# Optimization experiments

Hardware: AMD Instinct MI355X
Metric: run time of the kernel (lower is better)

## Reference

```python
import jax, jax.numpy as jnp
import numpy as np

NEG = -9e15
ALPHA = 0.2  # leaky relu slope

def setup_inputs() -> dict:
    key = jax.random.key(0)
    k1, k2, k3, k4 = jax.random.split(key, 4)
    N, Fin, Fout = 8192, 512, 256
    h = jax.random.normal(k1, (N, Fin), dtype=jnp.float32)
    adj = jax.random.randint(k2, (N, N), 0, 2, dtype=jnp.int32)
    # xavier_uniform with gain=1.414
    gain = 1.414
    limW = gain * np.sqrt(6.0 / (Fin + Fout))
    W = jax.random.uniform(k3, (Fin, Fout), dtype=jnp.float32, minval=-limW, maxval=limW)
    lima = gain * np.sqrt(6.0 / (2 * Fout + 1))
    a = jax.random.uniform(k4, (2 * Fout, 1), dtype=jnp.float32, minval=-lima, maxval=lima)
    return {"h": h, "adj": adj, "W": W, "a": a}

def reference(h, adj, W, a):
    Fout = W.shape[1]
    Wh = h @ W                                   # [N, Fout]
    # decompose a = [a1; a2]: e_ij = leaky(a1.Wh_i + a2.Wh_j)
    f1 = Wh @ a[:Fout]                           # [N, 1]
    f2 = Wh @ a[Fout:]                           # [N, 1]
    e = jax.nn.leaky_relu(f1 + f2.T, negative_slope=ALPHA)  # [N, N]
    e = jnp.where(adj > 0, e, jnp.float32(NEG))
    attention = jax.nn.softmax(e, axis=1)
    # dropout is identity at inference (training=False)
    h_prime = attention @ Wh                     # [N, Fout]
    return jax.nn.elu(h_prime)
```

## Files before the change

### kernel.cpp

```cpp
#include <hip/hip_runtime.h>
#include <cstdint>
#include <cstddef>

#define ALPHA 0.2f

typedef __attribute__((ext_vector_type(8)))  short short8;
typedef __attribute__((ext_vector_type(16))) float f32x16;

static __device__ __forceinline__ unsigned short f2bf(float x) {
  union { float f; unsigned u; } c; c.f = x;
  unsigned u = c.u;
  unsigned r = (u + 0x7FFFu + ((u >> 16) & 1u)) >> 16;
  return (unsigned short)r;
}

__global__ __launch_bounds__(256, 2) void gemm1(const float* __restrict__ h,
                                                const float* __restrict__ W,
                                                float* __restrict__ Wh) {
  __shared__ float As[32][132];
  __shared__ float Bs[32][64];
  const int t = threadIdx.x;
  const int bid = blockIdx.x;
  const int nb = bid & 3, mb = bid >> 2;
  const int m0 = mb * 128, n0 = nb * 64;
  const int ty = t >> 4, tx = t & 15;
  float acc[8][4];
#pragma unroll
  for (int i = 0; i < 8; i++)
#pragma unroll
    for (int j = 0; j < 4; j++) acc[i][j] = 0.f;

  for (int k0 = 0; k0 < 512; k0 += 32) {
#pragma unroll
    for (int c = 0; c < 4; c++) {
      int m = c * 32 + (t >> 3);
      int kq = (t & 7) * 4;
      float4 v = *(const float4*)&h[(size_t)(m0 + m) * 512 + k0 + kq];
      As[kq + 0][m] = v.x; As[kq + 1][m] = v.y;
      As[kq + 2][m] = v.z; As[kq + 3][m] = v.w;
    }
#pragma unroll
    for (int c = 0; c < 2; c++) {
      int k = c * 16 + (t >> 4);
      int n = (t & 15) * 4;
      *(float4*)&Bs[k][n] = *(const float4*)&W[(size_t)(k0 + k) * 256 + n0 + n];
    }
    __syncthreads();
#pragma unroll
    for (int k = 0; k < 32; k++) {
      float4 a0 = *(float4*)&As[k][ty * 8];
      float4 a1 = *(float4*)&As[k][ty * 8 + 4];
      float4 b  = *(float4*)&Bs[k][tx * 4];
      float av[8] = {a0.x, a0.y, a0.z, a0.w, a1.x, a1.y, a1.z, a1.w};
      float bv[4] = {b.x, b.y, b.z, b.w};
#pragma unroll
      for (int i = 0; i < 8; i++)
#pragma unroll
        for (int j = 0; j < 4; j++) acc[i][j] = fmaf(av[i], bv[j], acc[i][j]);
    }
    __syncthreads();
  }
#pragma unroll
  for (int i = 0; i < 8; i++) {
    float4 v = {acc[i][0], acc[i][1], acc[i][2], acc[i][3]};
    *(float4*)&Wh[(size_t)(m0 + ty * 8 + i) * 256 + n0 + tx * 4] = v;
  }
}

__global__ __launch_bounds__(256) void rowstats(const float* __restrict__ Wh,
                                                const float* __restrict__ a,
                                                float* __restrict__ f1,
                                                float* __restrict__ f2,
                                                unsigned* __restrict__ uvpack) {
  const int t = threadIdx.x;
  const int w = t >> 6, lane = t & 63;
  const int i = blockIdx.x * 4 + w;
  float4 wv = *(const float4*)&Wh[(size_t)i * 256 + lane * 4];
  float4 a1 = *(const float4*)&a[lane * 4];
  float4 a2 = *(const float4*)&a[256 + lane * 4];
  float s1 = wv.x * a1.x + wv.y * a1.y + wv.z * a1.z + wv.w * a1.w;
  float s2 = wv.x * a2.x + wv.y * a2.y + wv.z * a2.z + wv.w * a2.w;
#pragma unroll
  for (int off = 32; off; off >>= 1) { s1 += __shfl_xor(s1, off); s2 += __shfl_xor(s2, off); }
  if (lane == 0) {
    f1[i] = s1; f2[i] = s2;
    float u = __expf(s2), v = __expf(ALPHA * s2);
    uvpack[i] = (unsigned)f2bf(u) | ((unsigned)f2bf(v) << 16);
  }
}

__global__ __launch_bounds__(256) void wtrans(const float* __restrict__ Wh,
                                              unsigned short* __restrict__ WhT) {
  __shared__ unsigned short T[64][80];
  const int t = threadIdx.x;
  const int bi = blockIdx.x & 127;
  const int bc = blockIdx.x >> 7;
  const int i0 = bi * 64, c0 = bc * 64;
  {
    const int il = t >> 2, cq = (t & 3) * 16;
#pragma unroll
    for (int k = 0; k < 4; ++k) {
      float4 v = *(const float4*)&Wh[(size_t)(i0 + il) * 256 + c0 + cq + k * 4];
      T[cq + k * 4 + 0][il] = f2bf(v.x);
      T[cq + k * 4 + 1][il] = f2bf(v.y);
      T[cq + k * 4 + 2][il] = f2bf(v.z);
      T[cq + k * 4 + 3][il] = f2bf(v.w);
    }
  }
  __syncthreads();
  {
    const int cl = t >> 2, iq = (t & 3) * 16;
    *(uint4*)&WhT[(size_t)(c0 + cl) * 8192 + i0 + iq]     = *(const uint4*)&T[cl][iq];
    *(uint4*)&WhT[(size_t)(c0 + cl) * 8192 + i0 + iq + 8] = *(const uint4*)&T[cl][iq + 8];
  }
}

__global__ __launch_bounds__(256) void f2max_k(const float* __restrict__ f2,
                                               float* __restrict__ f2maxp) {
  __shared__ float red[256];
  const int t = threadIdx.x;
  float m = -1e30f;
  for (int c = 0; c < 32; c++) m = fmaxf(m, f2[c * 256 + t]);
  red[t] = m;
  __syncthreads();
  for (int s = 128; s; s >>= 1) {
    if (t < s) red[t] = fmaxf(red[t], red[t + s]);
    __syncthreads();
  }
  if (t == 0) f2maxp[0] = red[0];
}

__global__ __launch_bounds__(256) void maskpack(const int* __restrict__ adj,
                                                unsigned long long* __restrict__ mask) {
  __shared__ unsigned long long mbuf[4][128];
  const int t = threadIdx.x, wave = t >> 6, lane = t & 63;
  const int row = blockIdx.x * 4 + wave;
  const int* ap = adj + (size_t)row * 8192 + lane;
#pragma unroll 1
  for (int it0 = 0; it0 < 128; it0 += 4) {
    int a0 = ap[(it0 + 0) * 64];
    int a1 = ap[(it0 + 1) * 64];
    int a2 = ap[(it0 + 2) * 64];
    int a3 = ap[(it0 + 3) * 64];
    unsigned long long b0 = __ballot(a0 > 0);
    unsigned long long b1 = __ballot(a1 > 0);
    unsigned long long b2 = __ballot(a2 > 0);
    unsigned long long b3 = __ballot(a3 > 0);
    if (lane == 0) {
      mbuf[wave][it0 + 0] = b0; mbuf[wave][it0 + 1] = b1;
      mbuf[wave][it0 + 2] = b2; mbuf[wave][it0 + 3] = b3;
    }
  }
  __syncthreads();
  uint4* dst = (uint4*)(mask + (size_t)blockIdx.x * 4 * 128);
  dst[t] = ((const uint4*)mbuf)[t];
}

#define ATTN_SUB(KSUB, MWORD, UCA, UCB, BFC, BFN, SCUR)                          \
  {                                                                              \
    const unsigned mbyte_ = ((MWORD) >> (((KSUB) & 1) * 16 + aselsh)) & 0xFFu;   \
    const unsigned uu_[8] = {UCA.x, UCA.y, UCA.z, UCA.w, UCB.x, UCB.y, UCB.z, UCB.w}; \
    float w_[8];                                                                 \
    _Pragma("unroll")                                                            \
    for (int jj = 0; jj < 8; jj++) {                                             \
      union { unsigned u; float f; } cu_, cv_;                                   \
      cu_.u = uu_[jj] << 16;                                                     \
      cv_.u = uu_[jj] & 0xFFFF0000u;                                             \
      float wv_ = (cu_.f > Ui) ? Ai * cu_.f : Bi * cv_.f;                        \
      int ext_ = ((int)(mbyte_ << (31 - jj))) >> 31;    \
      union { float f; int i; } wu_; wu_.f = wv_; wu_.i &= ext_;                 \
      w_[jj] = wu_.f;                                                            \
    }                                                                            \
    lpriv += ((w_[0] + w_[1]) + (w_[2] + w_[3])) + ((w_[4] + w_[5]) + (w_[6] + w_[7])); \
    union { uint4 q; short8 s; } af_;                                            \
    asm("v_cvt_pk_bf16_f32 %0, %1, %2" : "=v"(af_.q.x) : "v"(w_[0]), "v"(w_[1]));\
    asm("v_cvt_pk_bf16_f32 %0, %1, %2" : "=v"(af_.q.y) : "v"(w_[2]), "v"(w_[3]));\
    asm("v_cvt_pk_bf16_f32 %0, %1, %2" : "=v"(af_.q.z) : "v"(w_[4]), "v"(w_[5]));\
    asm("v_cvt_pk_bf16_f32 %0, %1, %2" : "=v"(af_.q.w) : "v"(w_[6]), "v"(w_[7]));\
    const int sn_ = (SCUR) + 1 < 128 ? (SCUR) + 1 : 127;                         \
    _Pragma("unroll")                                                            \
    for (int ct = 0; ct < 8; ct++)                                               \
      BFN[ct] = *(const short8*)(wtp + (size_t)ct * (32 * 8192) + (size_t)sn_ * 16); \
    _Pragma("unroll")                                                            \
    for (int ct = 0; ct < 8; ct++)                                               \
      acc[ct] = __builtin_amdgcn_mfma_f32_32x32x16_bf16(af_.s, BFC[ct], acc[ct], 0, 0, 0); \
  }

#define ATTN_GROUP(G, UC, UN, MC, MN)                                            \
  {                                                                              \
    const int gn_ = (G) < 31 ? (G) + 1 : 31;                                     \
    MN = mp[gn_];                                                                \
    UN[0] = *(const uint4*)(uvp + gn_ * 64 + 0);                                 \
    UN[1] = *(const uint4*)(uvp + gn_ * 64 + 4);                                 \
    ATTN_SUB(0, MC.x, UC[0], UC[1], bfA, bfB, 4 * (G) + 0);                      \
    UN[2] = *(const uint4*)(uvp + gn_ * 64 + 16);                                \
    UN[3] = *(const uint4*)(uvp + gn_ * 64 + 20);                                \
    ATTN_SUB(1, MC.x, UC[2], UC[3], bfB, bfA, 4 * (G) + 1);                      \
    UN[4] = *(const uint4*)(uvp + gn_ * 64 + 32);                                \
    UN[5] = *(const uint4*)(uvp + gn_ * 64 + 36);                                \
    ATTN_SUB(2, MC.y, UC[4], UC[5], bfA, bfB, 4 * (G) + 2);                      \
    UN[6] = *(const uint4*)(uvp + gn_ * 64 + 48);                                \
    UN[7] = *(const uint4*)(uvp + gn_ * 64 + 52);                                \
    ATTN_SUB(3, MC.y, UC[6], UC[7], bfB, bfA, 4 * (G) + 3);                      \
  }

__global__ __launch_bounds__(256, 1) void attn_main(const unsigned long long* __restrict__ maskw,
                                                    const float* __restrict__ f1,
                                                    const unsigned* __restrict__ uvpack,
                                                    const unsigned short* __restrict__ WhT,
                                                    const float* __restrict__ f2maxp,
                                                    float* __restrict__ out) {
  __shared__ float red[4][32][260];
  __shared__ float lsum[4][32];
  const int t = threadIdx.x;
  const int wave = t >> 6, lane = t & 63;
  const int am = lane & 31, asel = lane >> 5;
  const int aselsh = asel * 8;
  const int r0 = blockIdx.x * 32;
  const int row = r0 + am;
  const int jq = wave * 2048;

  const float F2max = f2maxp[0];
  const float f1v = f1[row];
  const float x = f1v + F2max;
  const float M = x > 0.f ? x : ALPHA * x;
  const float Ai = __expf(f1v - M);
  const float Bi = __expf(ALPHA * f1v - M);
  const float Ui = __expf(-f1v);

  f32x16 acc[8] = {};
  const uint2* mp = (const uint2*)maskw + (size_t)row * 128 + wave * 32;
  const unsigned* uvp = uvpack + jq + aselsh;
  const unsigned short* wtp = WhT + (size_t)am * 8192 + jq + aselsh;

  uint2 mg = mp[0], mgN;
  uint4 ug[8], ugN[8];
#pragma unroll
  for (int k = 0; k < 4; k++) {
    ug[2 * k]     = *(const uint4*)(uvp + k * 16);
    ug[2 * k + 1] = *(const uint4*)(uvp + k * 16 + 4);
  }
  short8 bfA[8], bfB[8];
#pragma unroll
  for (int ct = 0; ct < 8; ct++)
    bfA[ct] = *(const short8*)(wtp + (size_t)ct * (32 * 8192));
  float lpriv = 0.f;

#pragma unroll 1
  for (int gg = 0; gg < 16; ++gg) {
    ATTN_GROUP(2 * gg,     ug,  ugN, mg,  mgN);
    ATTN_GROUP(2 * gg + 1, ugN, ug,  mgN, mg);
  }

#pragma unroll
  for (int ct = 0; ct < 8; ct++) {
#pragma unroll
    for (int reg = 0; reg < 16; reg++) {
      const int rowl = (reg & 3) + 8 * (reg >> 2) + 4 * asel;
      red[wave][rowl][ct * 32 + am] = acc[ct][reg];
    }
  }
  lpriv += __shfl_xor(lpriv, 32);
  if (asel == 0) lsum[wave][am] = lpriv;
  __syncthreads();

  const int rr = t >> 3, cb = (t & 7) * 32;
  const float l = lsum[0][rr] + lsum[1][rr] + lsum[2][rr] + lsum[3][rr];
  const float inv = 1.0f / fmaxf(l, 1e-30f);
#pragma unroll
  for (int cc = 0; cc < 32; cc += 4) {
    float4 v;
    v.x = red[0][rr][cb + cc + 0] + red[1][rr][cb + cc + 0] + red[2][rr][cb + cc + 0] + red[3][rr][cb + cc + 0];
    v.y = red[0][rr][cb + cc + 1] + red[1][rr][cb + cc + 1] + red[2][rr][cb + cc + 1] + red[3][rr][cb + cc + 1];
    v.z = red[0][rr][cb + cc + 2] + red[1][rr][cb + cc + 2] + red[2][rr][cb + cc + 2] + red[3][rr][cb + cc + 2];
    v.w = red[0][rr][cb + cc + 3] + red[1][rr][cb + cc + 3] + red[2][rr][cb + cc + 3] + red[3][rr][cb + cc + 3];
    v.x *= inv; v.y *= inv; v.z *= inv; v.w *= inv;
    float4 o;
    o.x = v.x > 0.f ? v.x : __expf(v.x) - 1.f;
    o.y = v.y > 0.f ? v.y : __expf(v.y) - 1.f;
    o.z = v.z > 0.f ? v.z : __expf(v.z) - 1.f;
    o.w = v.w > 0.f ? v.w : __expf(v.w) - 1.f;
    *(float4*)&out[(size_t)(r0 + rr) * 256 + cb + cc] = o;
  }
}

extern "C" void kernel_launch(void* const* d_in, const int* in_sizes, int n_in,
                              void* d_out, int out_size, void* d_ws, size_t ws_size,
                              hipStream_t stream) {
  const float* h  = (const float*)d_in[0];
  const int* adj  = (const int*)d_in[1];
  const float* W  = (const float*)d_in[2];
  const float* a  = (const float*)d_in[3];
  float* out = (float*)d_out;
  char* ws = (char*)d_ws;

  float* Wh            = (float*)ws;
  unsigned long long* mask = (unsigned long long*)(ws + (size_t)(8u << 20));
  unsigned short* WhT  = (unsigned short*)(ws + (size_t)(16u << 20));
  float* f1            = (float*)(ws + (size_t)(20u << 20));
  float* f2            = (float*)(ws + (size_t)(20u << 20) + (32u << 10));
  unsigned* uvpack     = (unsigned*)(ws + (size_t)(20u << 20) + (64u << 10));
  float* f2maxp        = (float*)(ws + (size_t)(20u << 20) + (96u << 10));

  maskpack<<<2048, 256, 0, stream>>>(adj, mask);
  gemm1<<<256, 256, 0, stream>>>(h, W, Wh);
  rowstats<<<2048, 256, 0, stream>>>(Wh, a, f1, f2, uvpack);
  wtrans<<<512, 256, 0, stream>>>(Wh, WhT);
  f2max_k<<<1, 256, 0, stream>>>(f2, f2maxp);
  attn_main<<<256, 256, 0, stream>>>(mask, f1, uvpack, WhT, f2maxp, out);
}
```

Before: 553.6 us.

## Split attention work across waves by output columns instead of key ranges

Each wave now computes 64 output columns over the full 8192-key range instead of all 256 columns over a quarter of the keys. This removes the large LDS cross-wave reduction buffer, the __syncthreads, and the per-wave accumulator array, and writes outputs straight from registers. In exchange, every wave recomputes the masked softmax weights for all keys, quadrupling that ALU work and the mask/uv loads per block, and the output stores become scalar and less coalesced.

```diff
diff --git a/kernel.cpp b/kernel.cpp
--- a/kernel.cpp
+++ b/kernel.cpp
@@ -177,18 +177,16 @@
     asm("v_cvt_pk_bf16_f32 %0, %1, %2" : "=v"(af_.q.y) : "v"(w_[2]), "v"(w_[3]));\
     asm("v_cvt_pk_bf16_f32 %0, %1, %2" : "=v"(af_.q.z) : "v"(w_[4]), "v"(w_[5]));\
     asm("v_cvt_pk_bf16_f32 %0, %1, %2" : "=v"(af_.q.w) : "v"(w_[6]), "v"(w_[7]));\
-    const int sn_ = (SCUR) + 1 < 128 ? (SCUR) + 1 : 127;                         \
-    _Pragma("unroll")                                                            \
-    for (int ct = 0; ct < 8; ct++)                                               \
-      BFN[ct] = *(const short8*)(wtp + (size_t)ct * (32 * 8192) + (size_t)sn_ * 16); \
-    _Pragma("unroll")                                                            \
-    for (int ct = 0; ct < 8; ct++)                                               \
-      acc[ct] = __builtin_amdgcn_mfma_f32_32x32x16_bf16(af_.s, BFC[ct], acc[ct], 0, 0, 0); \
+    const int sn_ = (SCUR) + 1 < 512 ? (SCUR) + 1 : 511;                         \
+    BFN[0] = *(const short8*)(wtp0 + (size_t)sn_ * 16);                          \
+    BFN[1] = *(const short8*)(wtp1 + (size_t)sn_ * 16);                          \
+    acc0 = __builtin_amdgcn_mfma_f32_32x32x16_bf16(af_.s, BFC[0], acc0, 0, 0, 0);\
+    acc1 = __builtin_amdgcn_mfma_f32_32x32x16_bf16(af_.s, BFC[1], acc1, 0, 0, 0);\
   }
 
 #define ATTN_GROUP(G, UC, UN, MC, MN)                                            \
   {                                                                              \
-    const int gn_ = (G) < 31 ? (G) + 1 : 31;                                     \
+    const int gn_ = (G) < 127 ? (G) + 1 : 127;                                   \
     MN = mp[gn_];                                                                \
     UN[0] = *(const uint4*)(uvp + gn_ * 64 + 0);                                 \
     UN[1] = *(const uint4*)(uvp + gn_ * 64 + 4);                                 \
@@ -210,15 +208,12 @@
                                                     const unsigned short* __restrict__ WhT,
                                                     const float* __restrict__ f2maxp,
                                                     float* __restrict__ out) {
-  __shared__ float red[4][32][260];
-  __shared__ float lsum[4][32];
   const int t = threadIdx.x;
   const int wave = t >> 6, lane = t & 63;
   const int am = lane & 31, asel = lane >> 5;
   const int aselsh = asel * 8;
   const int r0 = blockIdx.x * 32;
   const int row = r0 + am;
-  const int jq = wave * 2048;
 
   const float F2max = f2maxp[0];
   const float f1v = f1[row];
@@ -228,10 +223,11 @@
   const float Bi = __expf(ALPHA * f1v - M);
   const float Ui = __expf(-f1v);
 
-  f32x16 acc[8] = {};
-  const uint2* mp = (const uint2*)maskw + (size_t)row * 128 + wave * 32;
-  const unsigned* uvp = uvpack + jq + aselsh;
-  const unsigned short* wtp = WhT + (size_t)am * 8192 + jq + aselsh;
+  f32x16 acc0 = {}, acc1 = {};
+  const uint2* mp = (const uint2*)maskw + (size_t)row * 128;
+  const unsigned* uvp = uvpack + aselsh;
+  const unsigned short* wtp0 = WhT + (size_t)(wave * 64 + am) * 8192 + aselsh;
+  const unsigned short* wtp1 = wtp0 + (size_t)32 * 8192;
 
   uint2 mg = mp[0], mgN;
   uint4 ug[8], ugN[8];
@@ -240,47 +236,30 @@
     ug[2 * k]     = *(const uint4*)(uvp + k * 16);
     ug[2 * k + 1] = *(const uint4*)(uvp + k * 16 + 4);
   }
-  short8 bfA[8], bfB[8];
-#pragma unroll
-  for (int ct = 0; ct < 8; ct++)
-    bfA[ct] = *(const short8*)(wtp + (size_t)ct * (32 * 8192));
+  short8 bfA[2], bfB[2];
+  bfA[0] = *(const short8*)(wtp0);
+  bfA[1] = *(const short8*)(wtp1);
   float lpriv = 0.f;
 
 #pragma unroll 1
-  for (int gg = 0; gg < 16; ++gg) {
+  for (int gg = 0; gg < 64; ++gg) {
     ATTN_GROUP(2 * gg,     ug,  ugN, mg,  mgN);
     ATTN_GROUP(2 * gg + 1, ugN, ug,  mgN, mg);
   }
 
-#pragma unroll
-  for (int ct = 0; ct < 8; ct++) {
-#pragma unroll
-    for (int reg = 0; reg < 16; reg++) {
-      const int rowl = (reg & 3) + 8 * (reg >> 2) + 4 * asel;
-      red[wave][rowl][ct * 32 + am] = acc[ct][reg];
-    }
-  }
   lpriv += __shfl_xor(lpriv, 32);
-  if (asel == 0) lsum[wave][am] = lpriv;
-  __syncthreads();
-
-  const int rr = t >> 3, cb = (t & 7) * 32;
-  const float l = lsum[0][rr] + lsum[1][rr] + lsum[2][rr] + lsum[3][rr];
-  const float inv = 1.0f / fmaxf(l, 1e-30f);
-#pragma unroll
-  for (int cc = 0; cc < 32; cc += 4) {
-    float4 v;
-    v.x = red[0][rr][cb + cc + 0] + red[1][rr][cb + cc + 0] + red[2][rr][cb + cc + 0] + red[3][rr][cb + cc + 0];
-    v.y = red[0][rr][cb + cc + 1] + red[1][rr][cb + cc + 1] + red[2][rr][cb + cc + 1] + red[3][rr][cb + cc + 1];
-    v.z = red[0][rr][cb + cc + 2] + red[1][rr][cb + cc + 2] + red[2][rr][cb + cc + 2] + red[3][rr][cb + cc + 2];
-    v.w = red[0][rr][cb + cc + 3] + red[1][rr][cb + cc + 3] + red[2][rr][cb + cc + 3] + red[3][rr][cb + cc + 3];
-    v.x *= inv; v.y *= inv; v.z *= inv; v.w *= inv;
-    float4 o;
-    o.x = v.x > 0.f ? v.x : __expf(v.x) - 1.f;
-    o.y = v.y > 0.f ? v.y : __expf(v.y) - 1.f;
-    o.z = v.z > 0.f ? v.z : __expf(v.z) - 1.f;
-    o.w = v.w > 0.f ? v.w : __expf(v.w) - 1.f;
-    *(float4*)&out[(size_t)(r0 + rr) * 256 + cb + cc] = o;
+
+#pragma unroll
+  for (int reg = 0; reg < 16; reg++) {
+    const int rowl = (reg & 3) + 8 * (reg >> 2) + 4 * asel;
+    const float l = __shfl(lpriv, rowl);
+    const float inv = 1.0f / fmaxf(l, 1e-30f);
+    float v0 = acc0[reg] * inv;
+    float v1 = acc1[reg] * inv;
+    float o0 = v0 > 0.f ? v0 : __expf(v0) - 1.f;
+    float o1 = v1 > 0.f ? v1 : __expf(v1) - 1.f;
+    out[(size_t)(r0 + rowl) * 256 + wave * 64 + am] = o0;
+    out[(size_t)(r0 + rowl) * 256 + wave * 64 + 32 + am] = o1;
   }
 }
 
```

Measured after the change: 621.6 us. 12.3% more time.
